# Optimization experiments

Hardware: AMD Instinct MI355X
Metric: run time of the kernel (lower is better)

## Reference

```python
import jax, jax.numpy as jnp
import numpy as np

B, S, H, L, NH, DH, V, FF, WD, W = 16, 512, 768, 12, 12, 64, 30522, 3072, 256, 255
T = S - 1


def layer_norm(x, s, b, eps=1e-12):
    m = jnp.mean(x, -1, keepdims=True)
    v = jnp.mean((x - m) ** 2, -1, keepdims=True)
    return (x - m) * jax.lax.rsqrt(v + eps) * s + b


def setup_inputs() -> dict:
    key = jax.random.key(0)
    ks = jax.random.split(key, 20)
    rng = np.random.RandomState(0)
    # ragged structure: words per sentence and wordpieces per word
    sent_lens = rng.randint(128, W + 1, size=B)
    token_lens = np.zeros((B, W), dtype=np.int32)
    for i in range(B):
        token_lens[i, : sent_lens[i]] = rng.randint(1, 3, size=sent_lens[i])
    bert_len = token_lens.sum(1)  # wordpieces per sentence (no CLS/SEP)
    attention_mask = (np.arange(S)[None, :] < (bert_len + 2)[:, None]).astype(np.int32)
    input_ids = rng.randint(0, V, size=(B, S)).astype(np.int32)
    sd = 0.02
    rn = lambda k, sh: jax.random.normal(k, sh, jnp.float32) * sd
    inp = {
        "input_ids": jnp.asarray(input_ids),
        "attention_mask": jnp.asarray(attention_mask),
        "token_lens": jnp.asarray(token_lens),
        "word_emb": rn(ks[0], (V, H)),
        "pos_emb": rn(ks[1], (S, H)),
        "type_emb": rn(ks[2], (2, H)),
        "emb_ln_s": jnp.ones((H,), jnp.float32),
        "emb_ln_b": jnp.zeros((H,), jnp.float32),
        "Wq": rn(ks[3], (L, H, H)), "bq": jnp.zeros((L, H), jnp.float32),
        "Wk": rn(ks[4], (L, H, H)), "bk": jnp.zeros((L, H), jnp.float32),
        "Wv": rn(ks[5], (L, H, H)), "bv": jnp.zeros((L, H), jnp.float32),
        "Wo": rn(ks[6], (L, H, H)), "bo": jnp.zeros((L, H), jnp.float32),
        "ln1_s": jnp.ones((L, H), jnp.float32), "ln1_b": jnp.zeros((L, H), jnp.float32),
        "W1": rn(ks[7], (L, H, FF)), "b1": jnp.zeros((L, FF), jnp.float32),
        "W2": rn(ks[8], (L, FF, H)), "b2": jnp.zeros((L, H), jnp.float32),
        "ln2_s": jnp.ones((L, H), jnp.float32), "ln2_b": jnp.zeros((L, H), jnp.float32),
        "proj_W": rn(ks[9], (H, WD)), "proj_b": jnp.zeros((WD,), jnp.float32),
    }
    return inp


def reference(input_ids, attention_mask, token_lens, word_emb, pos_emb, type_emb,
              emb_ln_s, emb_ln_b, Wq, bq, Wk, bk, Wv, bv, Wo, bo, ln1_s, ln1_b,
              W1, b1, W2, b2, ln2_s, ln2_b, proj_W, proj_b):
    # --- BERT embeddings ---
    h = word_emb[input_ids] + pos_emb[None, :, :] + type_emb[0][None, None, :]
    h = layer_norm(h, emb_ln_s, emb_ln_b)
    att_bias = (1.0 - attention_mask.astype(jnp.float32))[:, None, None, :] * -10000.0

    def block(h, p):
        wq, bq_, wk, bk_, wv, bv_, wo, bo_, l1s, l1b, w1, b1_, w2, b2_, l2s, l2b = p
        q = (h @ wq + bq_).reshape(B, S, NH, DH)
        k = (h @ wk + bk_).reshape(B, S, NH, DH)
        v = (h @ wv + bv_).reshape(B, S, NH, DH)
        scores = jnp.einsum('bqnd,bknd->bnqk', q, k) / np.float32(np.sqrt(DH)) + att_bias
        a = jax.nn.softmax(scores, axis=-1)
        ctx = jnp.einsum('bnqk,bknd->bqnd', a, v).reshape(B, S, H)
        h = layer_norm(h + ctx @ wo + bo_, l1s, l1b)
        f = jax.nn.gelu(h @ w1 + b1_, approximate=False) @ w2 + b2_
        h = layer_norm(h + f, l2s, l2b)
        return h, None

    h, _ = jax.lax.scan(block, h, (Wq, bq, Wk, bk, Wv, bv, Wo, bo, ln1_s, ln1_b,
                                   W1, b1, W2, b2, ln2_s, ln2_b))
    # drop [CLS], project to word_dims
    hid = h[:, 1:, :] @ proj_W + proj_b  # [B, T, WD]
    # --- ragged segment-mean merge (vectorized form of merge_embedding) ---
    cum = jnp.cumsum(token_lens, axis=1)  # [B, W]
    pos = jnp.arange(T)
    word_id = jnp.sum(pos[None, :, None] >= cum[:, None, :], axis=-1)  # token -> word
    valid = pos[None, :] < cum[:, -1][:, None]  # token within bert_len
    onehot = ((word_id[:, :, None] == jnp.arange(W)[None, None, :]) & valid[:, :, None]).astype(hid.dtype)
    sums = jnp.einsum('btw,btd->bwd', onehot, hid)  # [B, W, WD]
    means = sums / jnp.maximum(token_lens, 1)[:, :, None].astype(hid.dtype)
    word_masks = (token_lens > 0).astype(jnp.float32)  # [B, W]
    return means, word_masks
```

## Files before the change

### kernel.cpp

```cpp
#include <hip/hip_runtime.h>
#include <stdint.h>

#define B_ 16
#define S_ 512
#define H_ 768
#define L_ 12
#define NH_ 12
#define DH_ 64
#define FF_ 3072
#define WD_ 256
#define W_ 255
#define MTOK_ (B_*S_)
#define QKVN_ 2304
#define MPADR_ 128

typedef _Float16 f16;
typedef _Float16 f16x8 __attribute__((ext_vector_type(8)));
typedef _Float16 f16x4 __attribute__((ext_vector_type(4)));
typedef _Float16 f16x2 __attribute__((ext_vector_type(2)));
typedef float f32x4 __attribute__((ext_vector_type(4)));

#define SCHED_FENCE() __builtin_amdgcn_sched_barrier(0)

__device__ __forceinline__ float gelu_fast(float x) {
  float u = x * (1.0f + 0.044715f * x * x);
  float e = __expf(-1.5957691216f * u);
  return __fdividef(x, 1.0f + e);
}

__device__ __forceinline__ void gload16(const f16* g, f16* l) {
  __builtin_amdgcn_global_load_lds(
      (const __attribute__((address_space(1))) void*)g,
      (__attribute__((address_space(3))) void*)l, 16, 0, 0);
}

template<int BM, int BN, int ACT, int OUTF16, int BIAS, int QKVW, int SPLITK>
__global__ __launch_bounds__(256) void gemm2_k(
    const f16* __restrict__ A, const f16* __restrict__ Bm, void* __restrict__ Cv,
    const float* __restrict__ bias, f16* __restrict__ vTp,
    const int* __restrict__ rowmap, const int* __restrict__ meta,
    int lda, int ldb, int ldc, int K, float scale, long czoff)
{
  constexpr int MI = BM / 32;
  constexpr int NI = BN / 32;
  const int gx = gridDim.x;
  int flat = blockIdx.y * gx + blockIdx.x;
  const int nlive = (meta[1] / BM) * gx;
  if (flat >= nlive) return;
  {
    int q = nlive >> 3, r = nlive & 7;
    int xcd = flat & 7, idx = flat >> 3;
    flat = (xcd < r ? xcd * (q + 1) : r * (q + 1) + (xcd - r) * q) + idx;
  }
  const int row0 = (flat / gx) * BM;
  const int col0 = (flat % gx) * BN;
  const int z = (SPLITK > 1) ? blockIdx.z : 0;
  const int kc_len = K / SPLITK;
  A  += (size_t)z * kc_len;
  Bm += (size_t)z * kc_len;

  __shared__ __align__(16) f16 lA[BM * 64];
  __shared__ __align__(16) f16 lB[BN * 64];
  const int lane = threadIdx.x & 63;
  const int wave = threadIdx.x >> 6;
  const int wr = wave >> 1, wc = wave & 1;
  const int srow = lane >> 3;
  const int scol = lane & 7;
  const int cs = scol ^ srow;

  int arow[BM / 32];
#pragma unroll
  for (int i = 0; i < BM / 32; ++i)
    arow[i] = rowmap[row0 + (wave * (BM / 32) + i) * 8 + srow];

  f32x4 acc[MI][NI] = {};
  const int nt = kc_len >> 6;
  const int rl = lane & 15, g = lane >> 4;
  for (int t = 0; t < nt; ++t) {
    __syncthreads();
    const int k0 = t * 64;
#pragma unroll
    for (int i = 0; i < BM / 32; ++i) {
      int seg = wave * (BM / 32) + i;
      gload16(&A[(size_t)arow[i] * lda + k0 + cs * 8], &lA[seg * 512]);
    }
#pragma unroll
    for (int i = 0; i < BN / 32; ++i) {
      int seg = wave * (BN / 32) + i;
      gload16(&Bm[(size_t)(col0 + seg * 8 + srow) * ldb + k0 + cs * 8], &lB[seg * 512]);
    }
    __syncthreads();
#pragma unroll
    for (int c = 0; c < 2; ++c) {
      f16x8 af[MI], bf[NI];
#pragma unroll
      for (int mi = 0; mi < MI; ++mi) {
        int r = wr * (MI * 16) + mi * 16 + rl;
        int u = (c * 4 + g) ^ (r & 7);
        af[mi] = *(const f16x8*)&lA[r * 64 + u * 8];
      }
#pragma unroll
      for (int ni = 0; ni < NI; ++ni) {
        int r = wc * (NI * 16) + ni * 16 + rl;
        int u = (c * 4 + g) ^ (r & 7);
        bf[ni] = *(const f16x8*)&lB[r * 64 + u * 8];
      }
#pragma unroll
      for (int mi = 0; mi < MI; ++mi)
#pragma unroll
        for (int ni = 0; ni < NI; ++ni)
          acc[mi][ni] = __builtin_amdgcn_mfma_f32_16x16x32_f16(af[mi], bf[ni], acc[mi][ni], 0, 0, 0);
    }
  }
  const int cl = lane & 15;
  const int rq = (lane >> 4) * 4;
#pragma unroll
  for (int mi = 0; mi < MI; ++mi) {
    const int4 rm4 = *(const int4*)&rowmap[row0 + wr * (MI * 16) + mi * 16 + rq];
    const int rows[4] = { rm4.x, rm4.y, rm4.z, rm4.w };
    const bool contig = (rm4.w == rm4.x + 3) && ((rm4.x & 3) == 0);
#pragma unroll
    for (int ni = 0; ni < NI; ++ni) {
      int col = col0 + wc * (NI * 16) + ni * 16 + cl;
      float bv = 0.f;
      if constexpr (BIAS) { if (SPLITK == 1 || z == 0) bv = bias[col]; }
      if constexpr (QKVW) {
        if (col >= 2 * H_) {
          int vc = col - 2 * H_;
          int h = vc >> 6, d = vc & 63;
          if (contig) {
            if (rm4.x < MTOK_) {
              int b = rm4.x >> 9, s = rm4.x & (S_ - 1);
              f16x4 o4;
#pragma unroll
              for (int r = 0; r < 4; ++r) o4[r] = (f16)(acc[mi][ni][r] * scale + bv);
              *(f16x4*)&vTp[(((size_t)(b * NH_ + h)) * DH_ + d) * S_ + s] = o4;
            }
          } else {
#pragma unroll
            for (int r = 0; r < 4; ++r) {
              int orow = rows[r];
              if (orow < MTOK_) {
                int b = orow >> 9, s = orow & (S_ - 1);
                vTp[(((size_t)(b * NH_ + h)) * DH_ + d) * S_ + s] = (f16)(acc[mi][ni][r] * scale + bv);
              }
            }
          }
          continue;
        }
      }
#pragma unroll
      for (int r = 0; r < 4; ++r) {
        float v = acc[mi][ni][r] * scale + bv;
        if constexpr (ACT == 1) v = gelu_fast(v);
        if constexpr (OUTF16) {
          ((f16*)Cv + (size_t)z * czoff)[(size_t)rows[r] * ldc + col] = (f16)v;
        } else {
          ((float*)Cv)[(size_t)rows[r] * ldc + col] = v;
        }
      }
    }
  }
}

__global__ __launch_bounds__(256) void fattn_k(
    const f16* __restrict__ qkv, const f16* __restrict__ vT,
    f16* __restrict__ ctx, const int* __restrict__ lenp)
{
  const int bh = blockIdx.x, qt = blockIdx.y;
  const int b = bh / NH_, h = bh - b * NH_;
  const int L = lenp[b];
  if ((qt << 7) >= L) return;
  const int nkt = (L + 63) >> 6;
  const int lane = threadIdx.x & 63, wave = threadIdx.x >> 6;
  const int rl = lane & 15, g = lane >> 4;
  const int srow = lane >> 3, scol = lane & 7;
  const int cs = scol ^ srow;

  __shared__ __align__(16) f16 lK[2][64 * 64];
  __shared__ __align__(16) f16 lV[2][64 * 64];
  __shared__ __align__(16) f16 lP[128 * 72];

  auto stage = [&](int p, int kt) {
#pragma unroll
    for (int i = 0; i < 2; ++i) {
      int seg = wave * 2 + i;
      int r = seg * 8 + srow;
      gload16(&qkv[((size_t)b * S_ + kt * 64 + r) * QKVN_ + H_ + h * DH_ + cs * 8], &lK[p][seg * 512]);
      gload16(&vT[((size_t)bh * DH_ + r) * S_ + kt * 64 + cs * 8], &lV[p][seg * 512]);
    }
  };

  const size_t qrow0 = (size_t)b * S_ + qt * 128 + wave * 32;
  f16x8 qf[2][2];
#pragma unroll
  for (int bq = 0; bq < 2; ++bq)
#pragma unroll
    for (int kc = 0; kc < 2; ++kc)
      qf[bq][kc] = *(const f16x8*)&qkv[(qrow0 + bq * 16 + rl) * QKVN_ + h * DH_ + kc * 32 + g * 8];

  float lsum[2] = {0.f, 0.f};
  f32x4 accO[2][4] = {};

  stage(0, 0);
  for (int kt = 0; kt < nkt; ++kt) {
    if (kt + 1 < nkt) {
      stage((kt + 1) & 1, kt + 1);
      asm volatile("s_waitcnt vmcnt(4) lgkmcnt(0)" ::: "memory");
    } else {
      asm volatile("s_waitcnt vmcnt(0) lgkmcnt(0)" ::: "memory");
    }
    SCHED_FENCE();
    __builtin_amdgcn_s_barrier();
    SCHED_FENCE();
    const int p = kt & 1;

    f32x4 accS[4][2] = {};
    __builtin_amdgcn_s_setprio(1);
#pragma unroll
    for (int kc = 0; kc < 2; ++kc) {
#pragma unroll
      for (int ak = 0; ak < 4; ++ak) {
        int row = ak * 16 + rl;
        int u = (kc * 4 + g) ^ (row & 7);
        f16x8 kf = *(const f16x8*)&lK[p][row * 64 + u * 8];
#pragma unroll
        for (int bq = 0; bq < 2; ++bq)
          accS[ak][bq] = __builtin_amdgcn_mfma_f32_16x16x32_f16(kf, qf[bq][kc], accS[ak][bq], 0, 0, 0);
      }
    }
    __builtin_amdgcn_s_setprio(0);

    const int kvb = kt * 64 + g * 4;
#pragma unroll
    for (int bq = 0; bq < 2; ++bq) {
      float pv[16];
      float ps = 0.f;
#pragma unroll
      for (int ak = 0; ak < 4; ++ak)
#pragma unroll
        for (int r = 0; r < 4; ++r) {
          float s = accS[ak][bq][r] * 0.125f;
          float pp = (kvb + ak * 16 + r < L) ? __expf(s) : 0.f;
          pv[ak * 4 + r] = pp;
          ps += pp;
        }
      ps += __shfl_xor(ps, 16);
      ps += __shfl_xor(ps, 32);
      lsum[bq] += ps;
      const int qrow = wave * 32 + bq * 16 + rl;
#pragma unroll
      for (int ak = 0; ak < 4; ++ak)
#pragma unroll
        for (int r2 = 0; r2 < 2; ++r2) {
          f16x2 pk = { (f16)pv[ak * 4 + r2 * 2], (f16)pv[ak * 4 + r2 * 2 + 1] };
          *(f16x2*)&lP[qrow * 72 + ak * 16 + g * 4 + r2 * 2] = pk;
        }
    }
    __builtin_amdgcn_s_setprio(1);
#pragma unroll
    for (int kc = 0; kc < 2; ++kc) {
      f16x8 pa[2], vf[4];
#pragma unroll
      for (int aq = 0; aq < 2; ++aq) {
        int prow = wave * 32 + aq * 16 + rl;
        pa[aq] = *(const f16x8*)&lP[prow * 72 + kc * 32 + g * 8];
      }
#pragma unroll
      for (int bd = 0; bd < 4; ++bd) {
        int vrow = bd * 16 + rl;
        int u = (kc * 4 + g) ^ (vrow & 7);
        vf[bd] = *(const f16x8*)&lV[p][vrow * 64 + u * 8];
      }
#pragma unroll
      for (int aq = 0; aq < 2; ++aq)
#pragma unroll
        for (int bd = 0; bd < 4; ++bd)
          accO[aq][bd] = __builtin_amdgcn_mfma_f32_16x16x32_f16(pa[aq], vf[bd], accO[aq][bd], 0, 0, 0);
    }
    __builtin_amdgcn_s_setprio(0);
    SCHED_FENCE();
    asm volatile("s_waitcnt lgkmcnt(0)" ::: "memory");
    SCHED_FENCE();
    __builtin_amdgcn_s_barrier();
    SCHED_FENCE();
  }

  float linv[2] = { 1.f / lsum[0], 1.f / lsum[1] };
  const size_t orow0 = (size_t)b * S_ + qt * 128 + wave * 32;
#pragma unroll
  for (int aq = 0; aq < 2; ++aq)
#pragma unroll
    for (int r = 0; r < 4; ++r) {
      float li = __shfl(linv[aq], (lane & 48) | (g * 4 + r));
      int q = aq * 16 + g * 4 + r;
#pragma unroll
      for (int bd = 0; bd < 4; ++bd)
        ctx[(orow0 + q) * H_ + h * DH_ + bd * 16 + rl] = (f16)(accO[aq][bd][r] * li);
    }
}

template<typename TI>
__global__ __launch_bounds__(256) void transpose_f16_k(
    const TI* __restrict__ in, f16* __restrict__ out,
    int ldin, int ldout, long i1, long o1)
{
  const int z = blockIdx.z;
  in  += (size_t)z * i1;
  out += (size_t)z * o1;
  __shared__ float t[32][33];
  const int kt = blockIdx.y * 32, nt = blockIdx.x * 32;
  const int tx = threadIdx.x & 31, tg = threadIdx.x >> 5;
#pragma unroll
  for (int i = 0; i < 4; ++i) {
    int k = tg * 4 + i;
    t[k][tx] = (float)in[(size_t)(kt + k) * ldin + nt + tx];
  }
  __syncthreads();
#pragma unroll
  for (int i = 0; i < 4; ++i) {
    int n = tg * 4 + i;
    out[(size_t)(nt + n) * ldout + kt + tx] = (f16)t[tx][n];
  }
}

__global__ void bias_cat_k(const float* __restrict__ bq, const float* __restrict__ bk,
                           const float* __restrict__ bv, float* __restrict__ out) {
  const int l = blockIdx.y;
  const int j = blockIdx.x * 256 + threadIdx.x;
  float v = (j < H_) ? bq[l * H_ + j] : (j < 2 * H_) ? bk[l * H_ + j - H_] : bv[l * H_ + j - 2 * H_];
  out[l * QKVN_ + j] = v;
}

__global__ __launch_bounds__(256) void embed_ln_k(
    const int* __restrict__ ids, const float* __restrict__ wemb,
    const float* __restrict__ pemb, const float* __restrict__ temb,
    const float* __restrict__ lns, const float* __restrict__ lnb,
    f16* __restrict__ h16)
{
  const int row = blockIdx.x * 4 + (threadIdx.x >> 6);
  const int lane = threadIdx.x & 63;
  const int s = row & (S_ - 1);
  const float4* wp = (const float4*)(wemb + (size_t)ids[row] * H_);
  const float4* pp = (const float4*)(pemb + (size_t)s * H_);
  const float4* tp = (const float4*)temb;
  float4 x[3]; float sm = 0.f, sq = 0.f;
#pragma unroll
  for (int j = 0; j < 3; ++j) {
    int i4 = lane + 64 * j;
    float4 a = wp[i4], bb = pp[i4], c = tp[i4];
    float4 v; v.x = a.x + bb.x + c.x; v.y = a.y + bb.y + c.y;
    v.z = a.z + bb.z + c.z; v.w = a.w + bb.w + c.w;
    x[j] = v;
    sm += v.x + v.y + v.z + v.w;
    sq += v.x * v.x + v.y * v.y + v.z * v.z + v.w * v.w;
  }
#pragma unroll
  for (int o = 32; o > 0; o >>= 1) { sm += __shfl_xor(sm, o); sq += __shfl_xor(sq, o); }
  float mean = sm * (1.f / H_);
  float inv = rsqrtf(sq * (1.f / H_) - mean * mean + 1e-12f);
  f16* ho = h16 + (size_t)row * H_;
#pragma unroll
  for (int j = 0; j < 3; ++j) {
    int i4 = lane + 64 * j;
    float4 sc = ((const float4*)lns)[i4], bi = ((const float4*)lnb)[i4];
    float4 v = x[j];
    f16x4 o4 = {(f16)((v.x - mean) * inv * sc.x + bi.x),
                (f16)((v.y - mean) * inv * sc.y + bi.y),
                (f16)((v.z - mean) * inv * sc.z + bi.z),
                (f16)((v.w - mean) * inv * sc.w + bi.w)};
    *(f16x4*)&ho[i4 * 4] = o4;
  }
}

__global__ __launch_bounds__(256) void ln_res_k(
    f16* __restrict__ h16, const f16* __restrict__ tmpA, const f16* __restrict__ tmpB,
    const float* __restrict__ lns, const float* __restrict__ lnb,
    const int* __restrict__ rowmap, const int* __restrict__ meta)
{
  const int crow = blockIdx.x * 4 + (threadIdx.x >> 6);
  if (crow >= meta[0]) return;
  const int row = rowmap[crow];
  const int lane = threadIdx.x & 63;
  const f16x4* hp = (const f16x4*)(h16 + (size_t)row * H_);
  const f16x4* ta = (const f16x4*)(tmpA + (size_t)row * H_);
  const f16x4* tb = (const f16x4*)(tmpB + (size_t)row * H_);
  float4 x[3]; float sm = 0.f, sq = 0.f;
#pragma unroll
  for (int j = 0; j < 3; ++j) {
    int i4 = lane + 64 * j;
    f16x4 a = hp[i4], va = ta[i4], vb = tb[i4];
    float4 v;
    v.x = (float)a[0] + (float)va[0] + (float)vb[0];
    v.y = (float)a[1] + (float)va[1] + (float)vb[1];
    v.z = (float)a[2] + (float)va[2] + (float)vb[2];
    v.w = (float)a[3] + (float)va[3] + (float)vb[3];
    x[j] = v;
    sm += v.x + v.y + v.z + v.w;
    sq += v.x * v.x + v.y * v.y + v.z * v.z + v.w * v.w;
  }
#pragma unroll
  for (int o = 32; o > 0; o >>= 1) { sm += __shfl_xor(sm, o); sq += __shfl_xor(sq, o); }
  float mean = sm * (1.f / H_);
  float inv = rsqrtf(sq * (1.f / H_) - mean * mean + 1e-12f);
  f16* ho = h16 + (size_t)row * H_;
#pragma unroll
  for (int j = 0; j < 3; ++j) {
    int i4 = lane + 64 * j;
    float4 sc = ((const float4*)lns)[i4], bi = ((const float4*)lnb)[i4];
    float4 v = x[j];
    f16x4 o4 = {(f16)((v.x - mean) * inv * sc.x + bi.x),
                (f16)((v.y - mean) * inv * sc.y + bi.y),
                (f16)((v.z - mean) * inv * sc.z + bi.z),
                (f16)((v.w - mean) * inv * sc.w + bi.w)};
    *(f16x4*)&ho[i4 * 4] = o4;
  }
}

__global__ void lenmap_k(const int* __restrict__ mask, int* __restrict__ len,
                         int* __restrict__ meta, int* __restrict__ rowmap) {
  const int t = threadIdx.x;
  __shared__ int red[512];
  __shared__ int cum[17];
  const int b = t >> 5, sl = t & 31;
  int part = 0;
#pragma unroll
  for (int j = 0; j < 16; ++j) part += mask[b * S_ + sl + 32 * j];
  red[t] = part; __syncthreads();
  for (int o = 16; o > 0; o >>= 1) {
    if (sl < o) red[t] += red[t + o];
    __syncthreads();
  }
  if (t == 0) {
    int c = 0; cum[0] = 0;
    for (int bb = 0; bb < B_; ++bb) { len[bb] = red[bb * 32]; c += red[bb * 32]; cum[bb + 1] = c; }
    meta[0] = c;
    meta[1] = (c + 127) & ~127;
  }
  __syncthreads();
  const int Mv = cum[16];
  for (int i = t; i < MTOK_ + MPADR_; i += 512) {
    int orig;
    if (i < Mv) {
      int bb = 0;
#pragma unroll
      for (int k = 1; k <= 16; ++k) bb += (i >= cum[k]) ? 1 : 0;
      orig = bb * S_ + (i - cum[bb]);
    } else {
      int d = i - Mv;
      orig = MTOK_ + (d < MPADR_ ? d : MPADR_ - 1);
    }
    rowmap[i] = orig;
  }
}

__global__ __launch_bounds__(256) void merge_k(
    const float* __restrict__ proj, const int* __restrict__ tl,
    float* __restrict__ means, float* __restrict__ masks)
{
  const int w = blockIdx.x, b = blockIdx.y;
  const int t = threadIdx.x;
  __shared__ int red[256];
  int part = 0;
  for (int j = t; j < w; j += 256) part += tl[b * W_ + j];
  red[t] = part; __syncthreads();
  for (int o = 128; o > 0; o >>= 1) { if (t < o) red[t] += red[t + o]; __syncthreads(); }
  const int start = red[0];
  const int len = tl[b * W_ + w];
  float s = 0.f;
  for (int l = 0; l < len; ++l)
    s += proj[((size_t)b * S_ + 1 + start + l) * WD_ + t];
  means[((size_t)b * W_ + w) * WD_ + t] = (len > 0) ? s / (float)len : 0.f;
  if (t == 0) masks[b * W_ + w] = (len > 0) ? 1.f : 0.f;
}

extern "C" void kernel_launch(void* const* d_in, const int* in_sizes, int n_in,
                              void* d_out, int out_size, void* d_ws, size_t ws_size,
                              hipStream_t stream)
{
  (void)in_sizes; (void)n_in; (void)out_size;
  const int*   ids   = (const int*)d_in[0];
  const int*   amask = (const int*)d_in[1];
  const int*   tlens = (const int*)d_in[2];
  const float* wemb  = (const float*)d_in[3];
  const float* pemb  = (const float*)d_in[4];
  const float* temb  = (const float*)d_in[5];
  const float* elns  = (const float*)d_in[6];
  const float* elnb  = (const float*)d_in[7];
  const float* Wq = (const float*)d_in[8];  const float* bq = (const float*)d_in[9];
  const float* Wk = (const float*)d_in[10]; const float* bk = (const float*)d_in[11];
  const float* Wv = (const float*)d_in[12]; const float* bv = (const float*)d_in[13];
  const float* Wo = (const float*)d_in[14]; const float* bo = (const float*)d_in[15];
  const float* l1s = (const float*)d_in[16]; const float* l1b = (const float*)d_in[17];
  const float* W1 = (const float*)d_in[18]; const float* b1 = (const float*)d_in[19];
  const float* W2 = (const float*)d_in[20]; const float* b2 = (const float*)d_in[21];
  const float* l2s = (const float*)d_in[22]; const float* l2b = (const float*)d_in[23];
  const float* pW = (const float*)d_in[24]; const float* pb = (const float*)d_in[25];

  const int MR = MTOK_ + MPADR_;
  char* ws = (char*)d_ws;
  size_t off = 0;
  auto alloc = [&](size_t n) { void* r = ws + off; off += (n + 255) & ~(size_t)255; return r; };
  f16*   h16   = (f16*)alloc((size_t)MR * H_ * 2);
  f16*   qkv   = (f16*)alloc((size_t)MR * QKVN_ * 2);
  f16*   ctx16 = (f16*)alloc((size_t)MR * H_ * 2);
  f16*   vT    = (f16*)alloc((size_t)B_ * NH_ * DH_ * S_ * 2);
  f16*   ff16  = (f16*)alloc((size_t)MR * FF_ * 2);
  f16*   tmp16 = (f16*)alloc((size_t)MR * H_ * 2 * 2);
  float* proj32 = (float*)alloc((size_t)MR * WD_ * 4);
  f16*   pwT   = (f16*)alloc((size_t)WD_ * H_ * 2);
  float* bqkv  = (float*)alloc((size_t)L_ * QKVN_ * 4);
  int*   lenb  = (int*)alloc(256);
  int*   meta  = (int*)alloc(256);
  int*   rowmap = (int*)alloc((size_t)MR * 4);
  f16*   tmp16b = tmp16 + (size_t)MR * H_;

  const size_t wqkv_sz = (size_t)QKVN_ * H_ * 2;
  const size_t wo_sz   = (size_t)H_ * H_ * 2;
  const size_t w1_sz   = (size_t)H_ * FF_ * 2;
  const size_t w2_sz   = (size_t)FF_ * H_ * 2;
  const size_t per_layer_w = wqkv_sz + wo_sz + w1_sz + w2_sz;
  const bool big = ws_size >= off + (size_t)L_ * per_layer_w + 8192;
  const int nz = big ? L_ : 1;
  f16* wqkv0 = (f16*)alloc((size_t)nz * wqkv_sz);
  f16* wo0   = (f16*)alloc((size_t)nz * wo_sz);
  f16* w10   = (f16*)alloc((size_t)nz * w1_sz);
  f16* w20   = (f16*)alloc((size_t)nz * w2_sz);

  lenmap_k<<<1, 512, 0, stream>>>(amask, lenb, meta, rowmap);
  embed_ln_k<<<MTOK_ / 4, 256, 0, stream>>>(ids, wemb, pemb, temb, elns, elnb, h16);
  transpose_f16_k<float><<<dim3(WD_/32, H_/32, 1), 256, 0, stream>>>(pW, pwT, WD_, H_, 0, 0);
  bias_cat_k<<<dim3(QKVN_/256, L_), 256, 0, stream>>>(bq, bk, bv, bqkv);

  if (big) {
    transpose_f16_k<float><<<dim3(H_/32, H_/32, L_), 256, 0, stream>>>(
        Wq, wqkv0,                   H_, H_, (long)H_*H_, (long)QKVN_*H_);
    transpose_f16_k<float><<<dim3(H_/32, H_/32, L_), 256, 0, stream>>>(
        Wk, wqkv0 + (size_t)H_*H_,   H_, H_, (long)H_*H_, (long)QKVN_*H_);
    transpose_f16_k<float><<<dim3(H_/32, H_/32, L_), 256, 0, stream>>>(
        Wv, wqkv0 + (size_t)2*H_*H_, H_, H_, (long)H_*H_, (long)QKVN_*H_);
    transpose_f16_k<float><<<dim3(H_/32, H_/32, L_), 256, 0, stream>>>(
        Wo, wo0, H_, H_, (long)H_*H_, (long)H_*H_);
    transpose_f16_k<float><<<dim3(FF_/32, H_/32, L_), 256, 0, stream>>>(
        W1, w10, FF_, H_, (long)H_*FF_, (long)H_*FF_);
    transpose_f16_k<float><<<dim3(H_/32, FF_/32, L_), 256, 0, stream>>>(
        W2, w20, H_, FF_, (long)FF_*H_, (long)FF_*H_);
  }

  for (int l = 0; l < L_; ++l) {
    f16* wqkv_l = wqkv0 + (size_t)(big ? l : 0) * QKVN_ * H_;
    f16* wo_l   = wo0   + (size_t)(big ? l : 0) * H_ * H_;
    f16* w1_l   = w10   + (size_t)(big ? l : 0) * H_ * FF_;
    f16* w2_l   = w20   + (size_t)(big ? l : 0) * FF_ * H_;
    if (!big) {
      transpose_f16_k<float><<<dim3(H_/32, H_/32, 1), 256, 0, stream>>>(
          Wq + (size_t)l*H_*H_, wqkv_l,                   H_, H_, 0, 0);
      transpose_f16_k<float><<<dim3(H_/32, H_/32, 1), 256, 0, stream>>>(
          Wk + (size_t)l*H_*H_, wqkv_l + (size_t)H_*H_,   H_, H_, 0, 0);
      transpose_f16_k<float><<<dim3(H_/32, H_/32, 1), 256, 0, stream>>>(
          Wv + (size_t)l*H_*H_, wqkv_l + (size_t)2*H_*H_, H_, H_, 0, 0);
      transpose_f16_k<float><<<dim3(H_/32, H_/32, 1), 256, 0, stream>>>(
          Wo + (size_t)l*H_*H_, wo_l, H_, H_, 0, 0);
      transpose_f16_k<float><<<dim3(FF_/32, H_/32, 1), 256, 0, stream>>>(
          W1 + (size_t)l*H_*FF_, w1_l, FF_, H_, 0, 0);
      transpose_f16_k<float><<<dim3(H_/32, FF_/32, 1), 256, 0, stream>>>(
          W2 + (size_t)l*FF_*H_, w2_l, H_, FF_, 0, 0);
    }
    gemm2_k<128,128,0,1,1,1,1><<<dim3(QKVN_/128, MTOK_/128, 1), 256, 0, stream>>>(
        h16, wqkv_l, qkv, bqkv + (size_t)l*QKVN_, vT, rowmap, meta, H_, H_, QKVN_, H_, 1.0f, 0);
    fattn_k<<<dim3(B_*NH_, S_/128), 256, 0, stream>>>(qkv, vT, ctx16, lenb);
    gemm2_k<64,64,0,1,1,0,2><<<dim3(H_/64, MTOK_/64, 2), 256, 0, stream>>>(
        ctx16, wo_l, tmp16, bo + (size_t)l*H_, nullptr, rowmap, meta, H_, H_, H_, H_, 1.0f, (long)MR * H_);
    ln_res_k<<<MTOK_/4, 256, 0, stream>>>(h16, tmp16, tmp16b, l1s + (size_t)l*H_, l1b + (size_t)l*H_, rowmap, meta);
    gemm2_k<128,128,1,1,1,0,1><<<dim3(FF_/128, MTOK_/128, 1), 256, 0, stream>>>(
        h16, w1_l, ff16, b1 + (size_t)l*FF_, nullptr, rowmap, meta, H_, H_, FF_, H_, 1.0f, 0);
    gemm2_k<64,64,0,1,1,0,2><<<dim3(H_/64, MTOK_/64, 2), 256, 0, stream>>>(
        ff16, w2_l, tmp16, b2 + (size_t)l*H_, nullptr, rowmap, meta, FF_, FF_, H_, FF_, 1.0f, (long)MR * H_);
    ln_res_k<<<MTOK_/4, 256, 0, stream>>>(h16, tmp16, tmp16b, l2s + (size_t)l*H_, l2b + (size_t)l*H_, rowmap, meta);
  }

  gemm2_k<64,64,0,0,1,0,1><<<dim3(WD_/64, MTOK_/64, 1), 256, 0, stream>>>(
      h16, pwT, proj32, pb, nullptr, rowmap, meta, H_, H_, WD_, H_, 1.0f, 0);
  merge_k<<<dim3(W_, B_), 256, 0, stream>>>(proj32, tlens,
      (float*)d_out, (float*)d_out + (size_t)B_ * W_ * WD_);
}
```

Baseline: 2.284 ms.

## Use compact row indexing in GEMMs, shrink attention query tile, fp16 projection output

```diff
diff --git a/kernel.cpp b/kernel.cpp
--- a/kernel.cpp
+++ b/kernel.cpp
@@ -34,7 +34,7 @@
       (__attribute__((address_space(3))) void*)l, 16, 0, 0);
 }
 
-template<int BM, int BN, int ACT, int OUTF16, int BIAS, int QKVW, int SPLITK>
+template<int BM, int BN, int ACT, int OUTF16, int BIAS, int QKVW, int SPLITK, int CIN, int COUT>
 __global__ __launch_bounds__(256) void gemm2_k(
     const f16* __restrict__ A, const f16* __restrict__ Bm, void* __restrict__ Cv,
     const float* __restrict__ bias, f16* __restrict__ vTp,
@@ -70,8 +70,10 @@
 
   int arow[BM / 32];
 #pragma unroll
-  for (int i = 0; i < BM / 32; ++i)
-    arow[i] = rowmap[row0 + (wave * (BM / 32) + i) * 8 + srow];
+  for (int i = 0; i < BM / 32; ++i) {
+    int cr = row0 + (wave * (BM / 32) + i) * 8 + srow;
+    arow[i] = CIN ? cr : rowmap[cr];
+  }
 
   f32x4 acc[MI][NI] = {};
   const int nt = kc_len >> 6;
@@ -116,9 +118,19 @@
   const int rq = (lane >> 4) * 4;
 #pragma unroll
   for (int mi = 0; mi < MI; ++mi) {
-    const int4 rm4 = *(const int4*)&rowmap[row0 + wr * (MI * 16) + mi * 16 + rq];
-    const int rows[4] = { rm4.x, rm4.y, rm4.z, rm4.w };
-    const bool contig = (rm4.w == rm4.x + 3) && ((rm4.x & 3) == 0);
+    const int crow0 = row0 + wr * (MI * 16) + mi * 16 + rq;
+    int rows[4];
+    bool contig;
+    if constexpr (COUT && !QKVW) {
+#pragma unroll
+      for (int r = 0; r < 4; ++r) rows[r] = crow0 + r;
+      contig = true;
+    } else {
+      const int4 rm4 = *(const int4*)&rowmap[crow0];
+      rows[0] = rm4.x; rows[1] = rm4.y; rows[2] = rm4.z; rows[3] = rm4.w;
+      contig = (rm4.w == rm4.x + 3) && ((rm4.x & 3) == 0);
+    }
+    (void)contig;
 #pragma unroll
     for (int ni = 0; ni < NI; ++ni) {
       int col = col0 + wc * (NI * 16) + ni * 16 + cl;
@@ -129,8 +141,8 @@
           int vc = col - 2 * H_;
           int h = vc >> 6, d = vc & 63;
           if (contig) {
-            if (rm4.x < MTOK_) {
-              int b = rm4.x >> 9, s = rm4.x & (S_ - 1);
+            if (rows[0] < MTOK_) {
+              int b = rows[0] >> 9, s = rows[0] & (S_ - 1);
               f16x4 o4;
 #pragma unroll
               for (int r = 0; r < 4; ++r) o4[r] = (f16)(acc[mi][ni][r] * scale + bv);
@@ -170,7 +182,7 @@
   const int bh = blockIdx.x, qt = blockIdx.y;
   const int b = bh / NH_, h = bh - b * NH_;
   const int L = lenp[b];
-  if ((qt << 7) >= L) return;
+  if ((qt << 6) >= L) return;
   const int nkt = (L + 63) >> 6;
   const int lane = threadIdx.x & 63, wave = threadIdx.x >> 6;
   const int rl = lane & 15, g = lane >> 4;
@@ -179,7 +191,7 @@
 
   __shared__ __align__(16) f16 lK[2][64 * 64];
   __shared__ __align__(16) f16 lV[2][64 * 64];
-  __shared__ __align__(16) f16 lP[128 * 72];
+  __shared__ __align__(16) f16 lP[64 * 72];
 
   auto stage = [&](int p, int kt) {
 #pragma unroll
@@ -191,16 +203,16 @@
     }
   };
 
-  const size_t qrow0 = (size_t)b * S_ + qt * 128 + wave * 32;
-  f16x8 qf[2][2];
-#pragma unroll
-  for (int bq = 0; bq < 2; ++bq)
-#pragma unroll
-    for (int kc = 0; kc < 2; ++kc)
-      qf[bq][kc] = *(const f16x8*)&qkv[(qrow0 + bq * 16 + rl) * QKVN_ + h * DH_ + kc * 32 + g * 8];
-
-  float lsum[2] = {0.f, 0.f};
-  f32x4 accO[2][4] = {};
+  const size_t qrow0 = (size_t)b * S_ + qt * 64 + wave * 16;
+  f16x8 qf[2];
+#pragma unroll
+  for (int kc = 0; kc < 2; ++kc) {
+    qf[kc] = *(const f16x8*)&qkv[(qrow0 + rl) * QKVN_ + h * DH_ + kc * 32 + g * 8];
+    qf[kc] *= (f16)0.125f;
+  }
+
+  float lsum = 0.f;
+  f32x4 accO[4] = {};
 
   stage(0, 0);
   for (int kt = 0; kt < nkt; ++kt) {
@@ -215,7 +227,7 @@
     SCHED_FENCE();
     const int p = kt & 1;
 
-    f32x4 accS[4][2] = {};
+    f32x4 accS[4] = {};
     __builtin_amdgcn_s_setprio(1);
 #pragma unroll
     for (int kc = 0; kc < 2; ++kc) {
@@ -224,31 +236,27 @@
         int row = ak * 16 + rl;
         int u = (kc * 4 + g) ^ (row & 7);
         f16x8 kf = *(const f16x8*)&lK[p][row * 64 + u * 8];
-#pragma unroll
-        for (int bq = 0; bq < 2; ++bq)
-          accS[ak][bq] = __builtin_amdgcn_mfma_f32_16x16x32_f16(kf, qf[bq][kc], accS[ak][bq], 0, 0, 0);
+        accS[ak] = __builtin_amdgcn_mfma_f32_16x16x32_f16(kf, qf[kc], accS[ak], 0, 0, 0);
       }
     }
     __builtin_amdgcn_s_setprio(0);
 
     const int kvb = kt * 64 + g * 4;
-#pragma unroll
-    for (int bq = 0; bq < 2; ++bq) {
+    {
       float pv[16];
       float ps = 0.f;
 #pragma unroll
       for (int ak = 0; ak < 4; ++ak)
 #pragma unroll
         for (int r = 0; r < 4; ++r) {
-          float s = accS[ak][bq][r] * 0.125f;
-          float pp = (kvb + ak * 16 + r < L) ? __expf(s) : 0.f;
+          float pp = (kvb + ak * 16 + r < L) ? __expf(accS[ak][r]) : 0.f;
           pv[ak * 4 + r] = pp;
           ps += pp;
         }
       ps += __shfl_xor(ps, 16);
       ps += __shfl_xor(ps, 32);
-      lsum[bq] += ps;
-      const int qrow = wave * 32 + bq * 16 + rl;
+      lsum += ps;
+      const int qrow = wave * 16 + rl;
 #pragma unroll
       for (int ak = 0; ak < 4; ++ak)
 #pragma unroll
@@ -260,12 +268,8 @@
     __builtin_amdgcn_s_setprio(1);
 #pragma unroll
     for (int kc = 0; kc < 2; ++kc) {
-      f16x8 pa[2], vf[4];
-#pragma unroll
-      for (int aq = 0; aq < 2; ++aq) {
-        int prow = wave * 32 + aq * 16 + rl;
-        pa[aq] = *(const f16x8*)&lP[prow * 72 + kc * 32 + g * 8];
-      }
+      f16x8 pa = *(const f16x8*)&lP[(wave * 16 + rl) * 72 + kc * 32 + g * 8];
+      f16x8 vf[4];
 #pragma unroll
       for (int bd = 0; bd < 4; ++bd) {
         int vrow = bd * 16 + rl;
@@ -273,10 +277,8 @@
         vf[bd] = *(const f16x8*)&lV[p][vrow * 64 + u * 8];
       }
 #pragma unroll
-      for (int aq = 0; aq < 2; ++aq)
-#pragma unroll
-        for (int bd = 0; bd < 4; ++bd)
-          accO[aq][bd] = __builtin_amdgcn_mfma_f32_16x16x32_f16(pa[aq], vf[bd], accO[aq][bd], 0, 0, 0);
+      for (int bd = 0; bd < 4; ++bd)
+        accO[bd] = __builtin_amdgcn_mfma_f32_16x16x32_f16(pa, vf[bd], accO[bd], 0, 0, 0);
     }
     __builtin_amdgcn_s_setprio(0);
     SCHED_FENCE();
@@ -286,18 +288,16 @@
     SCHED_FENCE();
   }
 
-  float linv[2] = { 1.f / lsum[0], 1.f / lsum[1] };
-  const size_t orow0 = (size_t)b * S_ + qt * 128 + wave * 32;
-#pragma unroll
-  for (int aq = 0; aq < 2; ++aq)
-#pragma unroll
-    for (int r = 0; r < 4; ++r) {
-      float li = __shfl(linv[aq], (lane & 48) | (g * 4 + r));
-      int q = aq * 16 + g * 4 + r;
-#pragma unroll
-      for (int bd = 0; bd < 4; ++bd)
-        ctx[(orow0 + q) * H_ + h * DH_ + bd * 16 + rl] = (f16)(accO[aq][bd][r] * li);
-    }
+  float linv = 1.f / lsum;
+  const size_t orow0 = (size_t)b * S_ + qt * 64 + wave * 16;
+#pragma unroll
+  for (int r = 0; r < 4; ++r) {
+    float li = __shfl(linv, (lane & 48) | (g * 4 + r));
+    int q = g * 4 + r;
+#pragma unroll
+    for (int bd = 0; bd < 4; ++bd)
+      ctx[(orow0 + q) * H_ + h * DH_ + bd * 16 + rl] = (f16)(accO[bd][r] * li);
+  }
 }
 
 template<typename TI>
@@ -383,8 +383,8 @@
   const int row = rowmap[crow];
   const int lane = threadIdx.x & 63;
   const f16x4* hp = (const f16x4*)(h16 + (size_t)row * H_);
-  const f16x4* ta = (const f16x4*)(tmpA + (size_t)row * H_);
-  const f16x4* tb = (const f16x4*)(tmpB + (size_t)row * H_);
+  const f16x4* ta = (const f16x4*)(tmpA + (size_t)crow * H_);
+  const f16x4* tb = (const f16x4*)(tmpB + (size_t)crow * H_);
   float4 x[3]; float sm = 0.f, sq = 0.f;
 #pragma unroll
   for (int j = 0; j < 3; ++j) {
@@ -455,7 +455,7 @@
 }
 
 __global__ __launch_bounds__(256) void merge_k(
-    const float* __restrict__ proj, const int* __restrict__ tl,
+    const f16* __restrict__ proj, const int* __restrict__ tl,
     float* __restrict__ means, float* __restrict__ masks)
 {
   const int w = blockIdx.x, b = blockIdx.y;
@@ -469,7 +469,7 @@
   const int len = tl[b * W_ + w];
   float s = 0.f;
   for (int l = 0; l < len; ++l)
-    s += proj[((size_t)b * S_ + 1 + start + l) * WD_ + t];
+    s += (float)proj[((size_t)b * S_ + 1 + start + l) * WD_ + t];
   means[((size_t)b * W_ + w) * WD_ + t] = (len > 0) ? s / (float)len : 0.f;
   if (t == 0) masks[b * W_ + w] = (len > 0) ? 1.f : 0.f;
 }
@@ -507,7 +507,7 @@
   f16*   vT    = (f16*)alloc((size_t)B_ * NH_ * DH_ * S_ * 2);
   f16*   ff16  = (f16*)alloc((size_t)MR * FF_ * 2);
   f16*   tmp16 = (f16*)alloc((size_t)MR * H_ * 2 * 2);
-  float* proj32 = (float*)alloc((size_t)MR * WD_ * 4);
+  f16*   projf = (f16*)alloc((size_t)MR * WD_ * 2);
   f16*   pwT   = (f16*)alloc((size_t)WD_ * H_ * 2);
   float* bqkv  = (float*)alloc((size_t)L_ * QKVN_ * 4);
   int*   lenb  = (int*)alloc(256);
@@ -566,21 +566,21 @@
       transpose_f16_k<float><<<dim3(H_/32, FF_/32, 1), 256, 0, stream>>>(
           W2 + (size_t)l*FF_*H_, w2_l, H_, FF_, 0, 0);
     }
-    gemm2_k<128,128,0,1,1,1,1><<<dim3(QKVN_/128, MTOK_/128, 1), 256, 0, stream>>>(
+    gemm2_k<128,128,0,1,1,1,1,0,0><<<dim3(QKVN_/128, MTOK_/128, 1), 256, 0, stream>>>(
         h16, wqkv_l, qkv, bqkv + (size_t)l*QKVN_, vT, rowmap, meta, H_, H_, QKVN_, H_, 1.0f, 0);
-    fattn_k<<<dim3(B_*NH_, S_/128), 256, 0, stream>>>(qkv, vT, ctx16, lenb);
-    gemm2_k<64,64,0,1,1,0,2><<<dim3(H_/64, MTOK_/64, 2), 256, 0, stream>>>(
+    fattn_k<<<dim3(B_*NH_, S_/64), 256, 0, stream>>>(qkv, vT, ctx16, lenb);
+    gemm2_k<64,64,0,1,1,0,2,0,1><<<dim3(H_/64, MTOK_/64, 2), 256, 0, stream>>>(
         ctx16, wo_l, tmp16, bo + (size_t)l*H_, nullptr, rowmap, meta, H_, H_, H_, H_, 1.0f, (long)MR * H_);
     ln_res_k<<<MTOK_/4, 256, 0, stream>>>(h16, tmp16, tmp16b, l1s + (size_t)l*H_, l1b + (size_t)l*H_, rowmap, meta);
-    gemm2_k<128,128,1,1,1,0,1><<<dim3(FF_/128, MTOK_/128, 1), 256, 0, stream>>>(
+    gemm2_k<128,128,1,1,1,0,1,0,1><<<dim3(FF_/128, MTOK_/128, 1), 256, 0, stream>>>(
         h16, w1_l, ff16, b1 + (size_t)l*FF_, nullptr, rowmap, meta, H_, H_, FF_, H_, 1.0f, 0);
-    gemm2_k<64,64,0,1,1,0,2><<<dim3(H_/64, MTOK_/64, 2), 256, 0, stream>>>(
+    gemm2_k<64,64,0,1,1,0,2,1,1><<<dim3(H_/64, MTOK_/64, 2), 256, 0, stream>>>(
         ff16, w2_l, tmp16, b2 + (size_t)l*H_, nullptr, rowmap, meta, FF_, FF_, H_, FF_, 1.0f, (long)MR * H_);
     ln_res_k<<<MTOK_/4, 256, 0, stream>>>(h16, tmp16, tmp16b, l2s + (size_t)l*H_, l2b + (size_t)l*H_, rowmap, meta);
   }
 
-  gemm2_k<64,64,0,0,1,0,1><<<dim3(WD_/64, MTOK_/64, 1), 256, 0, stream>>>(
-      h16, pwT, proj32, pb, nullptr, rowmap, meta, H_, H_, WD_, H_, 1.0f, 0);
-  merge_k<<<dim3(W_, B_), 256, 0, stream>>>(proj32, tlens,
+  gemm2_k<64,64,0,1,1,0,1,0,0><<<dim3(WD_/64, MTOK_/64, 1), 256, 0, stream>>>(
+      h16, pwT, projf, pb, nullptr, rowmap, meta, H_, H_, WD_, H_, 1.0f, 0);
+  merge_k<<<dim3(W_, B_), 256, 0, stream>>>(projf, tlens,
       (float*)d_out, (float*)d_out + (size_t)B_ * W_ * WD_);
 }
```

After: 2.259 ms. Within noise of the previous version (-1.1%).
